# Performance work log

Measured on AMD Instinct MI355X. Metric: run time of the kernel, lower is better.

## Reference

```python
import jax, jax.numpy as jnp
import numpy as np

N_NODES = 100000
N_EDGES = 1600000
IN_F = 512
OUT_F = 256
ORDER = 2


def setup_inputs() -> dict:
    key = jax.random.key(0)
    k1, k2, k3, k4, k5 = jax.random.split(key, 5)
    features = jax.random.normal(k1, (N_NODES, IN_F), dtype=jnp.float32)
    # Xavier-uniform init like torch.nn.init.xavier_uniform_
    limit = float(np.sqrt(6.0 / (IN_F + OUT_F)))
    weight = jax.random.uniform(k2, (IN_F, OUT_F), dtype=jnp.float32, minval=-limit, maxval=limit)
    row = jnp.sort(jax.random.randint(k3, (N_EDGES,), 0, N_NODES, dtype=jnp.int32))
    col = jax.random.randint(k4, (N_EDGES,), 0, N_NODES, dtype=jnp.int32)
    adj_vals = jax.random.uniform(k5, (N_EDGES,), dtype=jnp.float32)
    return {"features": features, "weight": weight, "row": row, "col": col, "adj_vals": adj_vals}


def _spmm(row, col, vals, x, n):
    # out[i] = sum_{e: row[e]==i} vals[e] * x[col[e]]  (COO sparse @ dense)
    msgs = vals[:, None] * x[col]  # [E, F]
    return jax.ops.segment_sum(msgs, row, num_segments=n)


def reference(features, weight, row, col, adj_vals):
    out = jnp.tanh(features @ weight)  # dense mm + tanh (active=True)
    for _ in range(ORDER):  # spmm once, then order-1 more times
        out = _spmm(row, col, adj_vals, out, N_NODES)
    return out
```

## Files before the change

kernel.cpp:

```cpp
#include <hip/hip_runtime.h>
#include <hip/hip_bf16.h>

#define M_NODES 100000
#define N_EDGES 1600000
#define K_IN 512
#define N_OUT 256

typedef short bf16x8 __attribute__((ext_vector_type(8)));
typedef float f32x4 __attribute__((ext_vector_type(4)));

__device__ inline unsigned short f2bf_u(float f) {
  union { float f; unsigned u; } x; x.f = f;
  unsigned r = x.u + 0x7FFFu + ((x.u >> 16) & 1u);
  return (unsigned short)(r >> 16);
}
__device__ inline float bfu2f(unsigned short h) {
  union { unsigned u; float f; } x; x.u = ((unsigned)h) << 16;
  return x.f;
}
__device__ inline float fast_tanh(float x) {
  float ax = __builtin_fabsf(x);
  float z = __expf(-2.0f * ax);
  float t = (1.0f - z) * __builtin_amdgcn_rcpf(1.0f + z);
  return __builtin_copysignf(t, x);
}
__device__ inline bf16x8 cvt8(float4 lo, float4 hi) {
  union { unsigned u[4]; bf16x8 v; } r;
  asm("v_cvt_pk_bf16_f32 %0, %1, %2" : "=v"(r.u[0]) : "v"(lo.x), "v"(lo.y));
  asm("v_cvt_pk_bf16_f32 %0, %1, %2" : "=v"(r.u[1]) : "v"(lo.z), "v"(lo.w));
  asm("v_cvt_pk_bf16_f32 %0, %1, %2" : "=v"(r.u[2]) : "v"(hi.x), "v"(hi.y));
  asm("v_cvt_pk_bf16_f32 %0, %1, %2" : "=v"(r.u[3]) : "v"(hi.z), "v"(hi.w));
  return r.v;
}

__global__ void prep_w_kernel(const float* __restrict__ w, short* __restrict__ wt) {
  int frag = blockIdx.x * 256 + threadIdx.x;
  int lane = frag & 63;
  int fi = frag >> 6;
  int ks = fi >> 4, nt = fi & 15;
  int quad = lane >> 4, l16 = lane & 15;
  int n = nt * 16 + l16;
  int k0 = ks * 32 + quad * 8;
  #pragma unroll
  for (int j = 0; j < 8; ++j)
    wt[(size_t)frag * 8 + j] = (short)f2bf_u(w[(size_t)(k0 + j) * N_OUT + n]);
}

__global__ void build_rp_kernel(const int* __restrict__ row, int* __restrict__ rp) {
  int r = blockIdx.x * 256 + threadIdx.x;
  if (r > M_NODES) return;
  int lo = 0, hi = N_EDGES;
  while (lo < hi) {
    int mid = (lo + hi) >> 1;
    if (row[mid] < r) lo = mid + 1; else hi = mid;
  }
  rp[r] = lo;
}

__global__ __launch_bounds__(64) void gemm_tanh_kernel(
    const float* __restrict__ A, const short* __restrict__ WtF,
    unsigned short* __restrict__ H) {
  const int lane = threadIdx.x;
  const int quad = lane >> 4, l16 = lane & 15;
  const int R0 = blockIdx.x * 32;

  f32x4 acc0[16], acc1[16];
  #pragma unroll
  for (int i = 0; i < 16; ++i) {
    acc0[i] = (f32x4){0.f, 0.f, 0.f, 0.f};
    acc1[i] = (f32x4){0.f, 0.f, 0.f, 0.f};
  }

  const float* Ab0 = A + (size_t)(R0 + l16) * K_IN + quad * 8;
  const float* Ab1 = Ab0 + (size_t)16 * K_IN;
  const short* Bb = WtF + lane * 8;

  float4 aA[4], aB[4];
  bf16x8 bP[8], bQ[8];

  aA[0] = *(const float4*)(Ab0);      aA[1] = *(const float4*)(Ab0 + 4);
  aA[2] = *(const float4*)(Ab1);      aA[3] = *(const float4*)(Ab1 + 4);
  aB[0] = *(const float4*)(Ab0 + 32); aB[1] = *(const float4*)(Ab0 + 36);
  aB[2] = *(const float4*)(Ab1 + 32); aB[3] = *(const float4*)(Ab1 + 36);
  #pragma unroll
  for (int nt = 0; nt < 8; ++nt)
    bP[nt] = *(const bf16x8*)(Bb + (size_t)nt * 512);
  #pragma unroll
  for (int nt = 0; nt < 8; ++nt)
    bQ[nt] = *(const bf16x8*)(Bb + (size_t)(8 + nt) * 512);

  #pragma unroll
  for (int p = 0; p < 8; ++p) {
    const int ks1 = 2 * p + 1;
    bf16x8 af0 = cvt8(aA[0], aA[1]);
    bf16x8 af1 = cvt8(aA[2], aA[3]);
    #pragma unroll
    for (int nt = 0; nt < 8; ++nt) {
      acc0[nt] = __builtin_amdgcn_mfma_f32_16x16x32_bf16(af0, bP[nt], acc0[nt], 0, 0, 0);
      acc1[nt] = __builtin_amdgcn_mfma_f32_16x16x32_bf16(af1, bP[nt], acc1[nt], 0, 0, 0);
    }
    #pragma unroll
    for (int nt = 0; nt < 8; ++nt)
      bP[nt] = *(const bf16x8*)(Bb + (size_t)(ks1 * 16 + nt) * 512);
    #pragma unroll
    for (int nt = 0; nt < 8; ++nt) {
      acc0[8 + nt] = __builtin_amdgcn_mfma_f32_16x16x32_bf16(af0, bQ[nt], acc0[8 + nt], 0, 0, 0);
      acc1[8 + nt] = __builtin_amdgcn_mfma_f32_16x16x32_bf16(af1, bQ[nt], acc1[8 + nt], 0, 0, 0);
    }
    #pragma unroll
    for (int nt = 0; nt < 8; ++nt)
      bQ[nt] = *(const bf16x8*)(Bb + (size_t)(ks1 * 16 + 8 + nt) * 512);
    bf16x8 ag0 = cvt8(aB[0], aB[1]);
    bf16x8 ag1 = cvt8(aB[2], aB[3]);
    if (p < 7) {
      __builtin_amdgcn_sched_barrier(0);
      const float* pa0 = Ab0 + (2 * p + 2) * 32;
      const float* pa1 = Ab1 + (2 * p + 2) * 32;
      aA[0] = *(const float4*)(pa0);      aA[1] = *(const float4*)(pa0 + 4);
      aA[2] = *(const float4*)(pa1);      aA[3] = *(const float4*)(pa1 + 4);
      aB[0] = *(const float4*)(pa0 + 32); aB[1] = *(const float4*)(pa0 + 36);
      aB[2] = *(const float4*)(pa1 + 32); aB[3] = *(const float4*)(pa1 + 36);
      __builtin_amdgcn_sched_barrier(0);
    }
    #pragma unroll
    for (int nt = 0; nt < 8; ++nt) {
      acc0[nt] = __builtin_amdgcn_mfma_f32_16x16x32_bf16(ag0, bP[nt], acc0[nt], 0, 0, 0);
      acc1[nt] = __builtin_amdgcn_mfma_f32_16x16x32_bf16(ag1, bP[nt], acc1[nt], 0, 0, 0);
    }
    #pragma unroll
    for (int nt = 0; nt < 8; ++nt) {
      acc0[8 + nt] = __builtin_amdgcn_mfma_f32_16x16x32_bf16(ag0, bQ[nt], acc0[8 + nt], 0, 0, 0);
      acc1[8 + nt] = __builtin_amdgcn_mfma_f32_16x16x32_bf16(ag1, bQ[nt], acc1[8 + nt], 0, 0, 0);
    }
    if (p < 7) {
      #pragma unroll
      for (int nt = 0; nt < 8; ++nt)
        bP[nt] = *(const bf16x8*)(Bb + (size_t)((ks1 + 1) * 16 + nt) * 512);
      #pragma unroll
      for (int nt = 0; nt < 8; ++nt)
        bQ[nt] = *(const bf16x8*)(Bb + (size_t)((ks1 + 1) * 16 + 8 + nt) * 512);
    }
  }

  #pragma unroll
  for (int nt = 0; nt < 16; ++nt) {
    #pragma unroll
    for (int rr = 0; rr < 4; ++rr) {
      int r0 = R0 + quad * 4 + rr;
      H[(size_t)r0 * N_OUT + nt * 16 + l16] = f2bf_u(fast_tanh(acc0[nt][rr]));
      H[(size_t)(r0 + 16) * N_OUT + nt * 16 + l16] = f2bf_u(fast_tanh(acc1[nt][rr]));
    }
  }
}

__global__ __launch_bounds__(256) void spmm_bf_bf(
    const int* __restrict__ rp, const int* __restrict__ colv,
    const float* __restrict__ vals, const unsigned short* __restrict__ x,
    unsigned short* __restrict__ y) {
  int w = (blockIdx.x * 256 + threadIdx.x) >> 6;
  int lane = threadIdx.x & 63;
  int i = __builtin_amdgcn_readfirstlane(w);
  int s = rp[i], e = rp[i + 1];
  float a0 = 0.f, a1 = 0.f, a2 = 0.f, a3 = 0.f;
  const unsigned short* xl = x + lane * 4;
  for (int base = s; base < e; base += 64) {
    int nn = min(e - base, 64);
    int tl = min(base + lane, e - 1);
    int c_l = colv[tl];
    float v_l = vals[tl];
    int tt = 0;
    for (; tt + 16 <= nn; tt += 16) {
      ushort4 xv[16]; float vv[16];
      #pragma unroll
      for (int j = 0; j < 16; ++j) {
        int c = __shfl(c_l, tt + j);
        vv[j] = __shfl(v_l, tt + j);
        xv[j] = *(const ushort4*)(xl + (size_t)c * N_OUT);
      }
      #pragma unroll
      for (int j = 0; j < 16; ++j) {
        a0 += vv[j] * bfu2f(xv[j].x); a1 += vv[j] * bfu2f(xv[j].y);
        a2 += vv[j] * bfu2f(xv[j].z); a3 += vv[j] * bfu2f(xv[j].w);
      }
    }
    for (; tt + 8 <= nn; tt += 8) {
      ushort4 xv[8]; float vv[8];
      #pragma unroll
      for (int j = 0; j < 8; ++j) {
        int c = __shfl(c_l, tt + j);
        vv[j] = __shfl(v_l, tt + j);
        xv[j] = *(const ushort4*)(xl + (size_t)c * N_OUT);
      }
      #pragma unroll
      for (int j = 0; j < 8; ++j) {
        a0 += vv[j] * bfu2f(xv[j].x); a1 += vv[j] * bfu2f(xv[j].y);
        a2 += vv[j] * bfu2f(xv[j].z); a3 += vv[j] * bfu2f(xv[j].w);
      }
    }
    for (; tt + 4 <= nn; tt += 4) {
      ushort4 xv[4]; float vv[4];
      #pragma unroll
      for (int j = 0; j < 4; ++j) {
        int c = __shfl(c_l, tt + j);
        vv[j] = __shfl(v_l, tt + j);
        xv[j] = *(const ushort4*)(xl + (size_t)c * N_OUT);
      }
      #pragma unroll
      for (int j = 0; j < 4; ++j) {
        a0 += vv[j] * bfu2f(xv[j].x); a1 += vv[j] * bfu2f(xv[j].y);
        a2 += vv[j] * bfu2f(xv[j].z); a3 += vv[j] * bfu2f(xv[j].w);
      }
    }
    for (; tt < nn; ++tt) {
      int c = __shfl(c_l, tt);
      float v = __shfl(v_l, tt);
      ushort4 xv = *(const ushort4*)(xl + (size_t)c * N_OUT);
      a0 += v * bfu2f(xv.x); a1 += v * bfu2f(xv.y);
      a2 += v * bfu2f(xv.z); a3 += v * bfu2f(xv.w);
    }
  }
  ushort4 o;
  o.x = f2bf_u(a0); o.y = f2bf_u(a1); o.z = f2bf_u(a2); o.w = f2bf_u(a3);
  *(ushort4*)(y + (size_t)i * N_OUT + lane * 4) = o;
}

__global__ __launch_bounds__(256) void spmm_bf_f32(
    const int* __restrict__ rp, const int* __restrict__ colv,
    const float* __restrict__ vals, const unsigned short* __restrict__ x,
    float* __restrict__ y) {
  int w = (blockIdx.x * 256 + threadIdx.x) >> 6;
  int lane = threadIdx.x & 63;
  int i = __builtin_amdgcn_readfirstlane(w);
  int s = rp[i], e = rp[i + 1];
  float a0 = 0.f, a1 = 0.f, a2 = 0.f, a3 = 0.f;
  const unsigned short* xl = x + lane * 4;
  for (int base = s; base < e; base += 64) {
    int nn = min(e - base, 64);
    int tl = min(base + lane, e - 1);
    int c_l = colv[tl];
    float v_l = vals[tl];
    int tt = 0;
    for (; tt + 16 <= nn; tt += 16) {
      ushort4 xv[16]; float vv[16];
      #pragma unroll
      for (int j = 0; j < 16; ++j) {
        int c = __shfl(c_l, tt + j);
        vv[j] = __shfl(v_l, tt + j);
        xv[j] = *(const ushort4*)(xl + (size_t)c * N_OUT);
      }
      #pragma unroll
      for (int j = 0; j < 16; ++j) {
        a0 += vv[j] * bfu2f(xv[j].x); a1 += vv[j] * bfu2f(xv[j].y);
        a2 += vv[j] * bfu2f(xv[j].z); a3 += vv[j] * bfu2f(xv[j].w);
      }
    }
    for (; tt + 8 <= nn; tt += 8) {
      ushort4 xv[8]; float vv[8];
      #pragma unroll
      for (int j = 0; j < 8; ++j) {
        int c = __shfl(c_l, tt + j);
        vv[j] = __shfl(v_l, tt + j);
        xv[j] = *(const ushort4*)(xl + (size_t)c * N_OUT);
      }
      #pragma unroll
      for (int j = 0; j < 8; ++j) {
        a0 += vv[j] * bfu2f(xv[j].x); a1 += vv[j] * bfu2f(xv[j].y);
        a2 += vv[j] * bfu2f(xv[j].z); a3 += vv[j] * bfu2f(xv[j].w);
      }
    }
    for (; tt + 4 <= nn; tt += 4) {
      ushort4 xv[4]; float vv[4];
      #pragma unroll
      for (int j = 0; j < 4; ++j) {
        int c = __shfl(c_l, tt + j);
        vv[j] = __shfl(v_l, tt + j);
        xv[j] = *(const ushort4*)(xl + (size_t)c * N_OUT);
      }
      #pragma unroll
      for (int j = 0; j < 4; ++j) {
        a0 += vv[j] * bfu2f(xv[j].x); a1 += vv[j] * bfu2f(xv[j].y);
        a2 += vv[j] * bfu2f(xv[j].z); a3 += vv[j] * bfu2f(xv[j].w);
      }
    }
    for (; tt < nn; ++tt) {
      int c = __shfl(c_l, tt);
      float v = __shfl(v_l, tt);
      ushort4 xv = *(const ushort4*)(xl + (size_t)c * N_OUT);
      a0 += v * bfu2f(xv.x); a1 += v * bfu2f(xv.y);
      a2 += v * bfu2f(xv.z); a3 += v * bfu2f(xv.w);
    }
  }
  float4 o = {a0, a1, a2, a3};
  *(float4*)(y + (size_t)i * N_OUT + lane * 4) = o;
}

extern "C" void kernel_launch(void* const* d_in, const int* in_sizes, int n_in,
                              void* d_out, int out_size, void* d_ws, size_t ws_size,
                              hipStream_t stream) {
  const float* features = (const float*)d_in[0];
  const float* weight   = (const float*)d_in[1];
  const int*   row      = (const int*)d_in[2];
  const int*   col      = (const int*)d_in[3];
  const float* vals     = (const float*)d_in[4];
  float* out = (float*)d_out;

  char* ws = (char*)d_ws;
  const size_t HB = (size_t)M_NODES * N_OUT * 2;
  const size_t RPB = 400016;
  unsigned short* H  = (unsigned short*)ws;
  unsigned short* y1 = (unsigned short*)(ws + HB);
  int*   rp = (int*)(ws + 2 * HB);
  short* Wt = (short*)(ws + 2 * HB + RPB);

  prep_w_kernel<<<64, 256, 0, stream>>>(weight, Wt);
  build_rp_kernel<<<(M_NODES + 1 + 255) / 256, 256, 0, stream>>>(row, rp);
  gemm_tanh_kernel<<<3125, 64, 0, stream>>>(features, Wt, H);
  spmm_bf_bf<<<25000, 256, 0, stream>>>(rp, col, vals, H, y1);
  spmm_bf_f32<<<25000, 256, 0, stream>>>(rp, col, vals, y1, out);
}
```

Baseline: 619.4 us.

## Restructure GEMM to 4-wave blocks with LDS double buffering via global_load_lds

The dense GEMM+tanh kernel moves from single-wave blocks of 32 rows, which each streamed the full weight matrix from global memory into registers, to 256-thread blocks of 64 rows. The A and B tiles are staged asynchronously into double-buffered LDS with direct global-to-LDS loads, and the A tile uses an XOR swizzle. The aim is to share weight reads across four waves and cut per-wave global traffic and register pressure. In exchange it adds a block barrier per k-step, uses more LDS per block, and gives each wave a smaller 64x64 output tile.

```diff
diff --git a/kernel.cpp b/kernel.cpp
--- a/kernel.cpp
+++ b/kernel.cpp
@@ -8,6 +8,9 @@
 
 typedef short bf16x8 __attribute__((ext_vector_type(8)));
 typedef float f32x4 __attribute__((ext_vector_type(4)));
+
+#define GLOBAL_AS __attribute__((address_space(1)))
+#define LDS_AS __attribute__((address_space(3)))
 
 __device__ inline unsigned short f2bf_u(float f) {
   union { float f; unsigned u; } x; x.f = f;
@@ -24,12 +27,12 @@
   float t = (1.0f - z) * __builtin_amdgcn_rcpf(1.0f + z);
   return __builtin_copysignf(t, x);
 }
-__device__ inline bf16x8 cvt8(float4 lo, float4 hi) {
+__device__ inline bf16x8 cvt8(f32x4 lo, f32x4 hi) {
   union { unsigned u[4]; bf16x8 v; } r;
-  asm("v_cvt_pk_bf16_f32 %0, %1, %2" : "=v"(r.u[0]) : "v"(lo.x), "v"(lo.y));
-  asm("v_cvt_pk_bf16_f32 %0, %1, %2" : "=v"(r.u[1]) : "v"(lo.z), "v"(lo.w));
-  asm("v_cvt_pk_bf16_f32 %0, %1, %2" : "=v"(r.u[2]) : "v"(hi.x), "v"(hi.y));
-  asm("v_cvt_pk_bf16_f32 %0, %1, %2" : "=v"(r.u[3]) : "v"(hi.z), "v"(hi.w));
+  asm("v_cvt_pk_bf16_f32 %0, %1, %2" : "=v"(r.u[0]) : "v"(lo[0]), "v"(lo[1]));
+  asm("v_cvt_pk_bf16_f32 %0, %1, %2" : "=v"(r.u[1]) : "v"(lo[2]), "v"(lo[3]));
+  asm("v_cvt_pk_bf16_f32 %0, %1, %2" : "=v"(r.u[2]) : "v"(hi[0]), "v"(hi[1]));
+  asm("v_cvt_pk_bf16_f32 %0, %1, %2" : "=v"(r.u[3]) : "v"(hi[2]), "v"(hi[3]));
   return r.v;
 }
 
@@ -57,98 +60,81 @@
   rp[r] = lo;
 }
 
-__global__ __launch_bounds__(64) void gemm_tanh_kernel(
+__global__ __launch_bounds__(256) void gemm_tanh_kernel(
     const float* __restrict__ A, const short* __restrict__ WtF,
     unsigned short* __restrict__ H) {
-  const int lane = threadIdx.x;
+  __shared__ __align__(16) float As[2][64 * 32];
+  __shared__ __align__(16) short Bs[2][256 * 32];
+  const int tid = threadIdx.x;
+  const int wave = tid >> 6, lane = tid & 63;
   const int quad = lane >> 4, l16 = lane & 15;
-  const int R0 = blockIdx.x * 32;
-
-  f32x4 acc0[16], acc1[16];
+  const int row0 = blockIdx.x * 64;
+
+  f32x4 acc[4][4];
   #pragma unroll
-  for (int i = 0; i < 16; ++i) {
-    acc0[i] = (f32x4){0.f, 0.f, 0.f, 0.f};
-    acc1[i] = (f32x4){0.f, 0.f, 0.f, 0.f};
-  }
-
-  const float* Ab0 = A + (size_t)(R0 + l16) * K_IN + quad * 8;
-  const float* Ab1 = Ab0 + (size_t)16 * K_IN;
-  const short* Bb = WtF + lane * 8;
-
-  float4 aA[4], aB[4];
-  bf16x8 bP[8], bQ[8];
-
-  aA[0] = *(const float4*)(Ab0);      aA[1] = *(const float4*)(Ab0 + 4);
-  aA[2] = *(const float4*)(Ab1);      aA[3] = *(const float4*)(Ab1 + 4);
-  aB[0] = *(const float4*)(Ab0 + 32); aB[1] = *(const float4*)(Ab0 + 36);
-  aB[2] = *(const float4*)(Ab1 + 32); aB[3] = *(const float4*)(Ab1 + 36);
+  for (int m = 0; m < 4; ++m)
+    #pragma unroll
+    for (int j = 0; j < 4; ++j) acc[m][j] = (f32x4){0.f, 0.f, 0.f, 0.f};
+
+  const int ar_lo = wave * 16 + (lane >> 3);
+  const int aswz = (lane & 7) ^ (lane >> 3);
+  const float* asrc0 = A + (size_t)min(row0 + ar_lo,     M_NODES - 1) * K_IN + aswz * 4;
+  const float* asrc1 = A + (size_t)min(row0 + ar_lo + 8, M_NODES - 1) * K_IN + aswz * 4;
+  const short* bsrc = WtF + (size_t)tid * 8;
+
+  #define STAGE(ks, b)                                                         \
+    do {                                                                       \
+      __builtin_amdgcn_global_load_lds(                                        \
+          (GLOBAL_AS const void*)(asrc0 + (ks) * 32),                          \
+          (LDS_AS void*)&As[b][(wave * 16 + 0) * 32], 16, 0, 0);               \
+      __builtin_amdgcn_global_load_lds(                                        \
+          (GLOBAL_AS const void*)(asrc1 + (ks) * 32),                          \
+          (LDS_AS void*)&As[b][(wave * 16 + 8) * 32], 16, 0, 0);               \
+      _Pragma("unroll")                                                        \
+      for (int i = 0; i < 4; ++i) {                                            \
+        __builtin_amdgcn_global_load_lds(                                      \
+            (GLOBAL_AS const void*)(bsrc + (size_t)(ks) * 8192 + i * 2048),    \
+            (LDS_AS void*)&Bs[b][(i * 256 + wave * 64) * 8], 16, 0, 0);        \
+      }                                                                        \
+    } while (0)
+
+  STAGE(0, 0);
+  __syncthreads();
+
+  int b = 0;
+  for (int ks = 0; ks < 16; ++ks) {
+    if (ks < 15) STAGE(ks + 1, b ^ 1);
+    bf16x8 bf[4];
+    #pragma unroll
+    for (int j = 0; j < 4; ++j)
+      bf[j] = *(const bf16x8*)&Bs[b][((wave * 4 + j) * 64 + lane) * 8];
+    #pragma unroll
+    for (int m = 0; m < 4; ++m) {
+      int row = m * 16 + l16;
+      f32x4 lo = *(const f32x4*)&As[b][row * 32 + (((quad * 2 + 0) ^ (l16 & 7)) * 4)];
+      f32x4 hi = *(const f32x4*)&As[b][row * 32 + (((quad * 2 + 1) ^ (l16 & 7)) * 4)];
+      bf16x8 af = cvt8(lo, hi);
+      #pragma unroll
+      for (int j = 0; j < 4; ++j)
+        acc[m][j] = __builtin_amdgcn_mfma_f32_16x16x32_bf16(af, bf[j], acc[m][j], 0, 0, 0);
+    }
+    __syncthreads();
+    b ^= 1;
+  }
+  #undef STAGE
+
   #pragma unroll
-  for (int nt = 0; nt < 8; ++nt)
-    bP[nt] = *(const bf16x8*)(Bb + (size_t)nt * 512);
-  #pragma unroll
-  for (int nt = 0; nt < 8; ++nt)
-    bQ[nt] = *(const bf16x8*)(Bb + (size_t)(8 + nt) * 512);
-
-  #pragma unroll
-  for (int p = 0; p < 8; ++p) {
-    const int ks1 = 2 * p + 1;
-    bf16x8 af0 = cvt8(aA[0], aA[1]);
-    bf16x8 af1 = cvt8(aA[2], aA[3]);
-    #pragma unroll
-    for (int nt = 0; nt < 8; ++nt) {
-      acc0[nt] = __builtin_amdgcn_mfma_f32_16x16x32_bf16(af0, bP[nt], acc0[nt], 0, 0, 0);
-      acc1[nt] = __builtin_amdgcn_mfma_f32_16x16x32_bf16(af1, bP[nt], acc1[nt], 0, 0, 0);
-    }
-    #pragma unroll
-    for (int nt = 0; nt < 8; ++nt)
-      bP[nt] = *(const bf16x8*)(Bb + (size_t)(ks1 * 16 + nt) * 512);
-    #pragma unroll
-    for (int nt = 0; nt < 8; ++nt) {
-      acc0[8 + nt] = __builtin_amdgcn_mfma_f32_16x16x32_bf16(af0, bQ[nt], acc0[8 + nt], 0, 0, 0);
-      acc1[8 + nt] = __builtin_amdgcn_mfma_f32_16x16x32_bf16(af1, bQ[nt], acc1[8 + nt], 0, 0, 0);
-    }
-    #pragma unroll
-    for (int nt = 0; nt < 8; ++nt)
-      bQ[nt] = *(const bf16x8*)(Bb + (size_t)(ks1 * 16 + 8 + nt) * 512);
-    bf16x8 ag0 = cvt8(aB[0], aB[1]);
-    bf16x8 ag1 = cvt8(aB[2], aB[3]);
-    if (p < 7) {
-      __builtin_amdgcn_sched_barrier(0);
-      const float* pa0 = Ab0 + (2 * p + 2) * 32;
-      const float* pa1 = Ab1 + (2 * p + 2) * 32;
-      aA[0] = *(const float4*)(pa0);      aA[1] = *(const float4*)(pa0 + 4);
-      aA[2] = *(const float4*)(pa1);      aA[3] = *(const float4*)(pa1 + 4);
-      aB[0] = *(const float4*)(pa0 + 32); aB[1] = *(const float4*)(pa0 + 36);
-      aB[2] = *(const float4*)(pa1 + 32); aB[3] = *(const float4*)(pa1 + 36);
-      __builtin_amdgcn_sched_barrier(0);
-    }
-    #pragma unroll
-    for (int nt = 0; nt < 8; ++nt) {
-      acc0[nt] = __builtin_amdgcn_mfma_f32_16x16x32_bf16(ag0, bP[nt], acc0[nt], 0, 0, 0);
-      acc1[nt] = __builtin_amdgcn_mfma_f32_16x16x32_bf16(ag1, bP[nt], acc1[nt], 0, 0, 0);
-    }
-    #pragma unroll
-    for (int nt = 0; nt < 8; ++nt) {
-      acc0[8 + nt] = __builtin_amdgcn_mfma_f32_16x16x32_bf16(ag0, bQ[nt], acc0[8 + nt], 0, 0, 0);
-      acc1[8 + nt] = __builtin_amdgcn_mfma_f32_16x16x32_bf16(ag1, bQ[nt], acc1[8 + nt], 0, 0, 0);
-    }
-    if (p < 7) {
-      #pragma unroll
-      for (int nt = 0; nt < 8; ++nt)
-        bP[nt] = *(const bf16x8*)(Bb + (size_t)((ks1 + 1) * 16 + nt) * 512);
-      #pragma unroll
-      for (int nt = 0; nt < 8; ++nt)
-        bQ[nt] = *(const bf16x8*)(Bb + (size_t)((ks1 + 1) * 16 + 8 + nt) * 512);
-    }
-  }
-
-  #pragma unroll
-  for (int nt = 0; nt < 16; ++nt) {
+  for (int m = 0; m < 4; ++m) {
     #pragma unroll
     for (int rr = 0; rr < 4; ++rr) {
-      int r0 = R0 + quad * 4 + rr;
-      H[(size_t)r0 * N_OUT + nt * 16 + l16] = f2bf_u(fast_tanh(acc0[nt][rr]));
-      H[(size_t)(r0 + 16) * N_OUT + nt * 16 + l16] = f2bf_u(fast_tanh(acc1[nt][rr]));
+      int row = row0 + m * 16 + quad * 4 + rr;
+      if (row < M_NODES) {
+        #pragma unroll
+        for (int j = 0; j < 4; ++j) {
+          H[(size_t)row * N_OUT + wave * 64 + j * 16 + l16] =
+              f2bf_u(fast_tanh(acc[m][j][rr]));
+        }
+      }
     }
   }
 }
@@ -314,7 +300,7 @@
 
   prep_w_kernel<<<64, 256, 0, stream>>>(weight, Wt);
   build_rp_kernel<<<(M_NODES + 1 + 255) / 256, 256, 0, stream>>>(row, rp);
-  gemm_tanh_kernel<<<3125, 64, 0, stream>>>(features, Wt, H);
+  gemm_tanh_kernel<<<(M_NODES + 63) / 64, 256, 0, stream>>>(features, Wt, H);
   spmm_bf_bf<<<25000, 256, 0, stream>>>(rp, col, vals, H, y1);
   spmm_bf_f32<<<25000, 256, 0, stream>>>(rp, col, vals, y1, out);
 }
```

Result: faster. 582.1 us (-6.0%).
